# Optimization experiments

Measured on AMD Instinct MI355X. Metric: run time of the kernel, lower is better.

## Reference

```python
import jax, jax.numpy as jnp
import numpy as np

D_MODEL = 1024
NUM_HEADS = 16
LN_EPS = 1e-5


def setup_inputs() -> dict:
    key = jax.random.key(0)
    ks = jax.random.split(key, 8)
    d = D_MODEL
    x = jax.random.normal(ks[0], (8, 1024, d), dtype=jnp.float32)
    # nn.MultiheadAttention parameters (combined in_proj, out_proj)
    in_proj_w = jax.random.normal(ks[1], (3 * d, d), dtype=jnp.float32) / np.sqrt(d)
    in_proj_b = jnp.zeros((3 * d,), dtype=jnp.float32)
    out_proj_w = jax.random.normal(ks[2], (d, d), dtype=jnp.float32) / np.sqrt(d)
    out_proj_b = jnp.zeros((d,), dtype=jnp.float32)
    ln_w = jnp.ones((d,), dtype=jnp.float32)
    ln_b = jnp.zeros((d,), dtype=jnp.float32)
    time_decay = jnp.asarray(0.1, dtype=jnp.float32)
    return {"x": x, "time_decay": time_decay, "in_proj_w": in_proj_w,
            "in_proj_b": in_proj_b, "out_proj_w": out_proj_w,
            "out_proj_b": out_proj_b, "ln_w": ln_w, "ln_b": ln_b}


def reference(x, time_decay, in_proj_w, in_proj_b, out_proj_w, out_proj_b, ln_w, ln_b):
    B, S, d = x.shape
    H = NUM_HEADS
    hd = d // H
    # vectorized time-decay bias: -|time_decay| * |i - j|  (replaces nested loop)
    idx = jnp.arange(S, dtype=jnp.float32)
    attn_bias = -jnp.abs(time_decay) * jnp.abs(idx[:, None] - idx[None, :])  # [S,S]
    # combined QKV projection
    qkv = x @ in_proj_w.T + in_proj_b  # [B,S,3d]
    q, k, v = jnp.split(qkv, 3, axis=-1)
    q = q.reshape(B, S, H, hd)
    k = k.reshape(B, S, H, hd)
    v = v.reshape(B, S, H, hd)
    scale = 1.0 / np.sqrt(hd)
    scores = jnp.einsum('bqhd,bkhd->bhqk', q, k) * scale + attn_bias  # [B,H,S,S]
    weights = jax.nn.softmax(scores, axis=-1)
    attn = jnp.einsum('bhqk,bkhd->bqhd', weights, v).reshape(B, S, d)
    attn_out = attn @ out_proj_w.T + out_proj_b
    # need_weights=True with default average_attn_weights=True -> mean over heads
    attn_weights = jnp.mean(weights, axis=1)  # [B,S,S]
    # residual + LayerNorm
    y = x + attn_out
    mu = jnp.mean(y, axis=-1, keepdims=True)
    var = jnp.mean(jnp.square(y - mu), axis=-1, keepdims=True)
    out = (y - mu) / jnp.sqrt(var + LN_EPS) * ln_w + ln_b
    return (out, attn_weights)
```

## Files before the change

kernel.cpp:

```cpp
#include <hip/hip_runtime.h>
#include <cstddef>

#define BATCH   8
#define SEQ     1024
#define DMODEL  1024
#define NHEAD   16
#define HDIM    64
#define D3      3072
#define NROWS   (BATCH * SEQ)
#define LN_EPS  1e-5f

typedef __attribute__((ext_vector_type(4))) float f32x4;
typedef __attribute__((ext_vector_type(8))) short bf16x8;

__device__ __forceinline__ float b2f(unsigned short u) {
    union { unsigned int i; float f; } v; v.i = ((unsigned int)u) << 16; return v.f;
}
__device__ __forceinline__ unsigned short f2bu(float f) {
    union { float f; unsigned int i; } v; v.f = f;
    unsigned int r = v.i + 0x7fffu + ((v.i >> 16) & 1u);
    return (unsigned short)(r >> 16);
}
__device__ __forceinline__ void gl16(const void* g, void* l) {
    __builtin_amdgcn_global_load_lds(
        (const __attribute__((address_space(1))) unsigned int*)g,
        (__attribute__((address_space(3))) unsigned int*)l, 16, 0, 0);
}

#define NG_X  1048576
#define NG_WQ 393216
#define NG_WO 131072
__global__ __launch_bounds__(256)
void cvt_bf16(const float* __restrict__ x, const float* __restrict__ wq,
              const float* __restrict__ wo,
              unsigned short* __restrict__ xb, unsigned short* __restrict__ wqb,
              unsigned short* __restrict__ wob) {
    const int gidx = blockIdx.x * 256 + threadIdx.x;
    const float* src; unsigned short* dst; size_t off;
    if (gidx < NG_X)              { src = x;  dst = xb;  off = (size_t)gidx * 8; }
    else if (gidx < NG_X + NG_WQ) { src = wq; dst = wqb; off = (size_t)(gidx - NG_X) * 8; }
    else                          { src = wo; dst = wob; off = (size_t)(gidx - NG_X - NG_WQ) * 8; }
    float4 v0 = *(const float4*)(src + off);
    float4 v1 = *(const float4*)(src + off + 4);
    uint4 pv;
    pv.x = f2bu(v0.x) | ((unsigned int)f2bu(v0.y) << 16);
    pv.y = f2bu(v0.z) | ((unsigned int)f2bu(v0.w) << 16);
    pv.z = f2bu(v1.x) | ((unsigned int)f2bu(v1.y) << 16);
    pv.w = f2bu(v1.z) | ((unsigned int)f2bu(v1.w) << 16);
    *(uint4*)(dst + off) = pv;
}

__global__ __launch_bounds__(256)
void qkv_mfma(const unsigned short* __restrict__ xb,
              const unsigned short* __restrict__ wb,
              const float* __restrict__ bias,
              unsigned short* __restrict__ qh,
              unsigned short* __restrict__ kh,
              unsigned short* __restrict__ vt) {
    __shared__ unsigned short smem[8192];
    unsigned short* As = smem;
    unsigned short* Bs = smem + 4096;

    const int t = threadIdx.x;
    const int w = t >> 6, lane = t & 63;
    const int wm = w >> 1, wn = w & 1;
    const int g = lane >> 4, c = lane & 15;
    const int m0 = blockIdx.y * 128, n0 = blockIdx.x * 128;

    const int srow = t >> 2;
    const int scol = (t & 3) * 8;
    const unsigned short* ga = xb + (size_t)(m0 + srow) * 1024 + scol;
    const unsigned short* gb = wb + (size_t)(n0 + srow) * 1024 + scol;

    f32x4 acc[4][4];
#pragma unroll
    for (int i = 0; i < 4; ++i)
#pragma unroll
        for (int j = 0; j < 4; ++j) acc[i][j] = (f32x4){0.f, 0.f, 0.f, 0.f};

    for (int k0 = 0; k0 < 1024; k0 += 32) {
        gl16(ga + k0,             As + t * 8);
        gl16(ga + 64 * 1024 + k0, As + 2048 + t * 8);
        gl16(gb + k0,             Bs + t * 8);
        gl16(gb + 64 * 1024 + k0, Bs + 2048 + t * 8);
        __syncthreads();
        bf16x8 af[4], bf[4];
#pragma unroll
        for (int i = 0; i < 4; ++i)
            af[i] = *(const bf16x8*)(As + (wm * 64 + i * 16 + c) * 32 + g * 8);
#pragma unroll
        for (int j = 0; j < 4; ++j)
            bf[j] = *(const bf16x8*)(Bs + (wn * 64 + j * 16 + c) * 32 + g * 8);
#pragma unroll
        for (int i = 0; i < 4; ++i)
#pragma unroll
            for (int j = 0; j < 4; ++j)
                acc[i][j] = __builtin_amdgcn_mfma_f32_16x16x32_bf16(af[i], bf[j], acc[i][j], 0, 0, 0);
        __syncthreads();
    }

    float bsv[4];
#pragma unroll
    for (int j = 0; j < 4; ++j) bsv[j] = bias[n0 + wn * 64 + j * 16 + c];

    unsigned short* eslice = smem + w * 2048;
    const int b_ = m0 >> 10;

    if (n0 < 2048) {
        const int ncl   = n0 + wn * 64;
        unsigned short* dst = (ncl < 1024)
            ? qh + ((size_t)(b_ * 16 + (ncl >> 6)) * 1024) * 64
            : kh + ((size_t)(b_ * 16 + ((ncl - 1024) >> 6)) * 1024) * 64;
#pragma unroll
        for (int half = 0; half < 2; ++half) {
#pragma unroll
            for (int ii = 0; ii < 2; ++ii) {
                const int i = half * 2 + ii;
#pragma unroll
                for (int j = 0; j < 4; ++j)
#pragma unroll
                    for (int r = 0; r < 4; ++r)
                        eslice[(ii * 16 + g * 4 + r) * 64 + j * 16 + c] = f2bu(acc[i][j][r] + bsv[j]);
            }
#pragma unroll
            for (int u = 0; u < 4; ++u) {
                const int mloc = u * 8 + (lane >> 3);
                const int ncol = (lane & 7) * 8;
                bf16x8 row = *(const bf16x8*)(eslice + mloc * 64 + ncol);
                const int tok = (m0 & 1023) + wm * 64 + half * 32 + mloc;
                *(bf16x8*)(dst + (size_t)tok * 64 + ncol) = row;
            }
        }
    } else {
        const int key0  = (m0 & 1023) + wm * 64;
        const int hbase = (n0 + wn * 64 - 2048) >> 6;
#pragma unroll
        for (int half = 0; half < 2; ++half) {
#pragma unroll
            for (int jj = 0; jj < 2; ++jj) {
                const int j = half * 2 + jj;
                const int nloc = jj * 16 + c;
#pragma unroll
                for (int i = 0; i < 4; ++i)
#pragma unroll
                    for (int r = 0; r < 4; ++r) {
                        const int mloc  = i * 16 + g * 4 + r;
                        const int mphys = mloc ^ ((nloc & 7) << 3);
                        eslice[nloc * 64 + mphys] = f2bu(acc[i][j][r] + bsv[j]);
                    }
            }
#pragma unroll
            for (int u = 0; u < 4; ++u) {
                const int nloc  = u * 8 + (lane >> 3);
                const int mb    = lane & 7;
                const int mphys = (mb ^ (nloc & 7)) * 8;
                bf16x8 row = *(const bf16x8*)(eslice + nloc * 64 + mphys);
                const int d = half * 32 + nloc;
                *(bf16x8*)(vt + ((size_t)((b_ * 16 + hbase) * 64 + d)) * 1024 + key0 + mb * 8) = row;
            }
        }
    }
}

__global__ __launch_bounds__(256, 4)
void attn_mfma(const unsigned short* __restrict__ qh,
               const unsigned short* __restrict__ kh,
               const unsigned short* __restrict__ vt,
               const float* __restrict__ tdp,
               unsigned short* __restrict__ attnb,
               float* __restrict__ wout) {
    const int qt = blockIdx.x;
    const int b  = blockIdx.y;
    const int hg = blockIdx.z;
    const int t  = threadIdx.x;
    const int w  = t >> 6;
    const int lane = t & 63;
    const int g  = lane >> 4;
    const int c  = lane & 15;

    const int q0 = qt * 16;
    const float td = -fabsf(tdp[0]);

    __shared__ unsigned short P_s[16][1032];
    __shared__ float rs_s[4][16];

    float wsum[16][4];
#pragma unroll
    for (int tt = 0; tt < 16; ++tt)
#pragma unroll
        for (int r = 0; r < 4; ++r) wsum[tt][r] = 0.f;

    const int key_base = w * 256;

    for (int hi = 0; hi < 8; ++hi) {
        const int h = hg * 8 + hi;
        const unsigned short* qslab = qh + (size_t)(b * 16 + h) * 1024 * 64;
        const unsigned short* kslab = kh + (size_t)(b * 16 + h) * 1024 * 64;

        bf16x8 qa0 = *(const bf16x8*)(qslab + (size_t)(q0 + c) * 64 + g * 8);
        bf16x8 qa1 = *(const bf16x8*)(qslab + (size_t)(q0 + c) * 64 + 32 + g * 8);

        float rsum[4] = {0.f, 0.f, 0.f, 0.f};
#pragma unroll 2
        for (int tt = 0; tt < 16; ++tt) {
            const int key = key_base + tt * 16 + c;
            const unsigned short* kp = kslab + (size_t)key * 64 + g * 8;
            bf16x8 kb0 = *(const bf16x8*)(kp);
            bf16x8 kb1 = *(const bf16x8*)(kp + 32);
            f32x4 z = {0.f, 0.f, 0.f, 0.f};
            z = __builtin_amdgcn_mfma_f32_16x16x32_bf16(qa0, kb0, z, 0, 0, 0);
            z = __builtin_amdgcn_mfma_f32_16x16x32_bf16(qa1, kb1, z, 0, 0, 0);
            const float kf = (float)key;
#pragma unroll
            for (int r = 0; r < 4; ++r) {
                const float qf = (float)(q0 + g * 4 + r);
                const float e = __expf(z[r] * 0.125f + td * fabsf(kf - qf));
                rsum[r] += e;
                P_s[g * 4 + r][key_base + tt * 16 + c] = f2bu(e);
            }
        }
#pragma unroll
        for (int r = 0; r < 4; ++r) {
            rsum[r] += __shfl_xor(rsum[r], 1, 64);
            rsum[r] += __shfl_xor(rsum[r], 2, 64);
            rsum[r] += __shfl_xor(rsum[r], 4, 64);
            rsum[r] += __shfl_xor(rsum[r], 8, 64);
        }
        if (c == 0) {
#pragma unroll
            for (int r = 0; r < 4; ++r) rs_s[w][g * 4 + r] = rsum[r];
        }
        __syncthreads();

        float invl[4];
#pragma unroll
        for (int r = 0; r < 4; ++r) {
            const int row = g * 4 + r;
            invl[r] = 1.0f / (rs_s[0][row] + rs_s[1][row] + rs_s[2][row] + rs_s[3][row]);
        }

        f32x4 accO = {0.f, 0.f, 0.f, 0.f};
        const unsigned short* vhp = vt + (size_t)((b * 16 + h) * 64 + w * 16 + c) * 1024;
#pragma unroll 8
        for (int ks = 0; ks < 32; ++ks) {
            bf16x8 pa = *(const bf16x8*)(&P_s[c][ks * 32 + g * 8]);
            bf16x8 vb = *(const bf16x8*)(vhp + ks * 32 + g * 8);
            accO = __builtin_amdgcn_mfma_f32_16x16x32_bf16(pa, vb, accO, 0, 0, 0);
        }
        unsigned short* op = attnb + (size_t)(b * 1024 + q0) * 1024 + h * 64 + w * 16 + c;
#pragma unroll
        for (int r = 0; r < 4; ++r)
            op[(size_t)(g * 4 + r) * 1024] = f2bu(accO[r] * invl[r]);

#pragma unroll
        for (int tt = 0; tt < 16; ++tt)
#pragma unroll
            for (int r = 0; r < 4; ++r)
                wsum[tt][r] += b2f(P_s[g * 4 + r][key_base + tt * 16 + c]) * invl[r];
        __syncthreads();
    }

#pragma unroll
    for (int tt = 0; tt < 16; ++tt) {
#pragma unroll
        for (int r = 0; r < 4; ++r) {
            atomicAdd(&wout[(size_t)(b * 1024 + q0 + g * 4 + r) * 1024 + key_base + tt * 16 + c],
                      wsum[tt][r] * (1.0f / NHEAD));
        }
    }
}

__global__ __launch_bounds__(256)
void outproj_mfma(const unsigned short* __restrict__ ab,
                  const unsigned short* __restrict__ wob,
                  const float* __restrict__ bias,
                  const float* __restrict__ X,
                  float* __restrict__ Y) {
    __shared__ unsigned short smem[8192];
    unsigned short* As = smem;
    unsigned short* Bs = smem + 4096;

    const int t = threadIdx.x;
    const int w = t >> 6, lane = t & 63;
    const int wm = w >> 1, wn = w & 1;
    const int g = lane >> 4, c = lane & 15;
    const int m0 = blockIdx.y * 128, n0 = blockIdx.x * 128;

    const int srow = t >> 2;
    const int scol = (t & 3) * 8;
    const unsigned short* ga = ab  + (size_t)(m0 + srow) * 1024 + scol;
    const unsigned short* gb = wob + (size_t)(n0 + srow) * 1024 + scol;

    f32x4 acc[4][4];
#pragma unroll
    for (int i = 0; i < 4; ++i)
#pragma unroll
        for (int j = 0; j < 4; ++j) acc[i][j] = (f32x4){0.f, 0.f, 0.f, 0.f};

    for (int k0 = 0; k0 < 1024; k0 += 32) {
        gl16(ga + k0,             As + t * 8);
        gl16(ga + 64 * 1024 + k0, As + 2048 + t * 8);
        gl16(gb + k0,             Bs + t * 8);
        gl16(gb + 64 * 1024 + k0, Bs + 2048 + t * 8);
        __syncthreads();
        bf16x8 af[4], bf[4];
#pragma unroll
        for (int i = 0; i < 4; ++i)
            af[i] = *(const bf16x8*)(As + (wm * 64 + i * 16 + c) * 32 + g * 8);
#pragma unroll
        for (int j = 0; j < 4; ++j)
            bf[j] = *(const bf16x8*)(Bs + (wn * 64 + j * 16 + c) * 32 + g * 8);
#pragma unroll
        for (int i = 0; i < 4; ++i)
#pragma unroll
            for (int j = 0; j < 4; ++j)
                acc[i][j] = __builtin_amdgcn_mfma_f32_16x16x32_bf16(af[i], bf[j], acc[i][j], 0, 0, 0);
        __syncthreads();
    }

    float bsv[4];
#pragma unroll
    for (int j = 0; j < 4; ++j) bsv[j] = bias[n0 + wn * 64 + j * 16 + c];

#pragma unroll
    for (int i = 0; i < 4; ++i) {
#pragma unroll
        for (int r = 0; r < 4; ++r) {
            const int m = m0 + wm * 64 + i * 16 + g * 4 + r;
#pragma unroll
            for (int j = 0; j < 4; ++j) {
                const int n = n0 + wn * 64 + j * 16 + c;
                Y[(size_t)m * 1024 + n] = acc[i][j][r] + bsv[j] + X[(size_t)m * 1024 + n];
            }
        }
    }
}

__global__ __launch_bounds__(256)
void ln_kernel(const float* __restrict__ Y, const float* __restrict__ lnw,
               const float* __restrict__ lnb, float* __restrict__ out) {
    const int row = blockIdx.x, t = threadIdx.x;
    __shared__ float rs[256], rq[256];
    const float4 v = ((const float4*)(Y + (size_t)row * DMODEL))[t];
    rs[t] = v.x + v.y + v.z + v.w;
    rq[t] = v.x * v.x + v.y * v.y + v.z * v.z + v.w * v.w;
    __syncthreads();
    for (int off = 128; off > 0; off >>= 1) {
        if (t < off) { rs[t] += rs[t + off]; rq[t] += rq[t + off]; }
        __syncthreads();
    }
    const float mu   = rs[0] * (1.0f / DMODEL);
    const float var  = rq[0] * (1.0f / DMODEL) - mu * mu;
    const float rstd = rsqrtf(var + LN_EPS);
    const float4 w  = ((const float4*)lnw)[t];
    const float4 bb = ((const float4*)lnb)[t];
    float4 o;
    o.x = (v.x - mu) * rstd * w.x + bb.x;
    o.y = (v.y - mu) * rstd * w.y + bb.y;
    o.z = (v.z - mu) * rstd * w.z + bb.z;
    o.w = (v.w - mu) * rstd * w.w + bb.w;
    ((float4*)(out + (size_t)row * DMODEL))[t] = o;
}

extern "C" void kernel_launch(void* const* d_in, const int* in_sizes, int n_in,
                              void* d_out, int out_size, void* d_ws, size_t ws_size,
                              hipStream_t stream) {
    (void)in_sizes; (void)n_in; (void)out_size; (void)ws_size;
    const float* x    = (const float*)d_in[0];
    const float* td   = (const float*)d_in[1];
    const float* wqkv = (const float*)d_in[2];
    const float* bqkv = (const float*)d_in[3];
    const float* wo   = (const float*)d_in[4];
    const float* bo   = (const float*)d_in[5];
    const float* lnw  = (const float*)d_in[6];
    const float* lnb  = (const float*)d_in[7];

    float* out_ln = (float*)d_out;
    float* out_w  = (float*)d_out + (size_t)NROWS * SEQ;

    unsigned short* qh = (unsigned short*)d_ws;
    unsigned short* kh = qh + (size_t)128 * 1024 * 64;
    unsigned short* vt = kh + (size_t)128 * 1024 * 64;
    float*          y  = (float*)d_ws;

    unsigned short* attnb = (unsigned short*)d_out;
    unsigned short* wob   = (unsigned short*)d_out + (size_t)NROWS * DMODEL;
    unsigned short* xb    = (unsigned short*)out_w;
    unsigned short* wqkvb = xb + (size_t)NROWS * DMODEL;

    cvt_bf16    <<<(NG_X + NG_WQ + NG_WO) / 256, 256, 0, stream>>>(x, wqkv, wo, xb, wqkvb, wob);
    qkv_mfma    <<<dim3(D3 / 128, NROWS / 128), 256, 0, stream>>>(xb, wqkvb, bqkv, qh, kh, vt);
    hipMemsetAsync(out_w, 0, (size_t)BATCH * SEQ * SEQ * sizeof(float), stream);
    attn_mfma   <<<dim3(SEQ / 16, BATCH, 2),    256, 0, stream>>>(qh, kh, vt, td, attnb, out_w);
    outproj_mfma<<<dim3(DMODEL / 128, NROWS / 128), 256, 0, stream>>>(attnb, wob, bo, x, y);
    ln_kernel   <<<NROWS,                       256, 0, stream>>>(y, lnw, lnb, out_ln);
}
```

Baseline: 511.3 us.

## Process 32 query rows per attention block to reuse K/V loads, use exp2

The attention kernel now handles two 16-row query tiles per block, so each K and V fragment loaded from global memory feeds two MFMAs. This halves the per-query K/V traffic and halves the grid size. Exp is replaced with the hardware exp2 intrinsic using pre-scaled constants. The cost is doubled register state (wsum grows to 128 floats) and doubled LDS for P_s, with launch bounds lowered from 4 to 2 blocks per SM, which reduces occupancy.

```diff
diff --git a/kernel.cpp b/kernel.cpp
--- a/kernel.cpp
+++ b/kernel.cpp
@@ -162,7 +162,7 @@
     }
 }
 
-__global__ __launch_bounds__(256, 4)
+__global__ __launch_bounds__(256, 2)
 void attn_mfma(const unsigned short* __restrict__ qh,
                const unsigned short* __restrict__ kh,
                const unsigned short* __restrict__ vt,
@@ -178,96 +178,131 @@
     const int g  = lane >> 4;
     const int c  = lane & 15;
 
-    const int q0 = qt * 16;
-    const float td = -fabsf(tdp[0]);
-
-    __shared__ unsigned short P_s[16][1032];
-    __shared__ float rs_s[4][16];
-
-    float wsum[16][4];
-#pragma unroll
-    for (int tt = 0; tt < 16; ++tt)
-#pragma unroll
-        for (int r = 0; r < 4; ++r) wsum[tt][r] = 0.f;
+    const int q0 = qt * 32;
+    const float td2 = -fabsf(tdp[0]) * 1.44269504f;
+    const float sc2 = 0.125f * 1.44269504f;
+
+    __shared__ unsigned short P_s[32][1032];
+    __shared__ float rs_s[4][32];
+
+    float wsum[2][16][4];
+#pragma unroll
+    for (int i = 0; i < 2; ++i)
+#pragma unroll
+        for (int tt = 0; tt < 16; ++tt)
+#pragma unroll
+            for (int r = 0; r < 4; ++r) wsum[i][tt][r] = 0.f;
 
     const int key_base = w * 256;
+    const float kf0 = (float)(key_base + c);
 
     for (int hi = 0; hi < 8; ++hi) {
         const int h = hg * 8 + hi;
         const unsigned short* qslab = qh + (size_t)(b * 16 + h) * 1024 * 64;
         const unsigned short* kslab = kh + (size_t)(b * 16 + h) * 1024 * 64;
 
-        bf16x8 qa0 = *(const bf16x8*)(qslab + (size_t)(q0 + c) * 64 + g * 8);
-        bf16x8 qa1 = *(const bf16x8*)(qslab + (size_t)(q0 + c) * 64 + 32 + g * 8);
-
-        float rsum[4] = {0.f, 0.f, 0.f, 0.f};
+        bf16x8 qa[2][2];
+#pragma unroll
+        for (int i = 0; i < 2; ++i) {
+            const unsigned short* qp = qslab + (size_t)(q0 + i * 16 + c) * 64 + g * 8;
+            qa[i][0] = *(const bf16x8*)(qp);
+            qa[i][1] = *(const bf16x8*)(qp + 32);
+        }
+
+        float rsum[2][4] = {{0.f,0.f,0.f,0.f},{0.f,0.f,0.f,0.f}};
 #pragma unroll 2
         for (int tt = 0; tt < 16; ++tt) {
             const int key = key_base + tt * 16 + c;
             const unsigned short* kp = kslab + (size_t)key * 64 + g * 8;
             bf16x8 kb0 = *(const bf16x8*)(kp);
             bf16x8 kb1 = *(const bf16x8*)(kp + 32);
-            f32x4 z = {0.f, 0.f, 0.f, 0.f};
-            z = __builtin_amdgcn_mfma_f32_16x16x32_bf16(qa0, kb0, z, 0, 0, 0);
-            z = __builtin_amdgcn_mfma_f32_16x16x32_bf16(qa1, kb1, z, 0, 0, 0);
-            const float kf = (float)key;
-#pragma unroll
-            for (int r = 0; r < 4; ++r) {
-                const float qf = (float)(q0 + g * 4 + r);
-                const float e = __expf(z[r] * 0.125f + td * fabsf(kf - qf));
-                rsum[r] += e;
-                P_s[g * 4 + r][key_base + tt * 16 + c] = f2bu(e);
-            }
-        }
-#pragma unroll
-        for (int r = 0; r < 4; ++r) {
-            rsum[r] += __shfl_xor(rsum[r], 1, 64);
-            rsum[r] += __shfl_xor(rsum[r], 2, 64);
-            rsum[r] += __shfl_xor(rsum[r], 4, 64);
-            rsum[r] += __shfl_xor(rsum[r], 8, 64);
-        }
+            f32x4 z0 = {0.f, 0.f, 0.f, 0.f};
+            f32x4 z1 = {0.f, 0.f, 0.f, 0.f};
+            z0 = __builtin_amdgcn_mfma_f32_16x16x32_bf16(qa[0][0], kb0, z0, 0, 0, 0);
+            z1 = __builtin_amdgcn_mfma_f32_16x16x32_bf16(qa[1][0], kb0, z1, 0, 0, 0);
+            z0 = __builtin_amdgcn_mfma_f32_16x16x32_bf16(qa[0][1], kb1, z0, 0, 0, 0);
+            z1 = __builtin_amdgcn_mfma_f32_16x16x32_bf16(qa[1][1], kb1, z1, 0, 0, 0);
+            const float kf = kf0 + (float)(tt * 16);
+#pragma unroll
+            for (int r = 0; r < 4; ++r) {
+                const float qf0 = (float)(q0 + g * 4 + r);
+                const float e0 = __builtin_amdgcn_exp2f(z0[r] * sc2 + td2 * fabsf(kf - qf0));
+                rsum[0][r] += e0;
+                P_s[g * 4 + r][key_base + tt * 16 + c] = f2bu(e0);
+                const float qf1 = qf0 + 16.0f;
+                const float e1 = __builtin_amdgcn_exp2f(z1[r] * sc2 + td2 * fabsf(kf - qf1));
+                rsum[1][r] += e1;
+                P_s[16 + g * 4 + r][key_base + tt * 16 + c] = f2bu(e1);
+            }
+        }
+#pragma unroll
+        for (int i = 0; i < 2; ++i)
+#pragma unroll
+            for (int r = 0; r < 4; ++r) {
+                rsum[i][r] += __shfl_xor(rsum[i][r], 1, 64);
+                rsum[i][r] += __shfl_xor(rsum[i][r], 2, 64);
+                rsum[i][r] += __shfl_xor(rsum[i][r], 4, 64);
+                rsum[i][r] += __shfl_xor(rsum[i][r], 8, 64);
+            }
         if (c == 0) {
 #pragma unroll
-            for (int r = 0; r < 4; ++r) rs_s[w][g * 4 + r] = rsum[r];
-        }
-        __syncthreads();
-
-        float invl[4];
-#pragma unroll
-        for (int r = 0; r < 4; ++r) {
-            const int row = g * 4 + r;
-            invl[r] = 1.0f / (rs_s[0][row] + rs_s[1][row] + rs_s[2][row] + rs_s[3][row]);
-        }
-
-        f32x4 accO = {0.f, 0.f, 0.f, 0.f};
+            for (int i = 0; i < 2; ++i)
+#pragma unroll
+                for (int r = 0; r < 4; ++r) rs_s[w][i * 16 + g * 4 + r] = rsum[i][r];
+        }
+        __syncthreads();
+
+        float invl[2][4];
+#pragma unroll
+        for (int i = 0; i < 2; ++i)
+#pragma unroll
+            for (int r = 0; r < 4; ++r) {
+                const int row = i * 16 + g * 4 + r;
+                invl[i][r] = 1.0f / (rs_s[0][row] + rs_s[1][row] + rs_s[2][row] + rs_s[3][row]);
+            }
+
+        f32x4 accO0 = {0.f, 0.f, 0.f, 0.f};
+        f32x4 accO1 = {0.f, 0.f, 0.f, 0.f};
         const unsigned short* vhp = vt + (size_t)((b * 16 + h) * 64 + w * 16 + c) * 1024;
-#pragma unroll 8
+#pragma unroll 4
         for (int ks = 0; ks < 32; ++ks) {
-            bf16x8 pa = *(const bf16x8*)(&P_s[c][ks * 32 + g * 8]);
-            bf16x8 vb = *(const bf16x8*)(vhp + ks * 32 + g * 8);
-            accO = __builtin_amdgcn_mfma_f32_16x16x32_bf16(pa, vb, accO, 0, 0, 0);
-        }
-        unsigned short* op = attnb + (size_t)(b * 1024 + q0) * 1024 + h * 64 + w * 16 + c;
-#pragma unroll
-        for (int r = 0; r < 4; ++r)
-            op[(size_t)(g * 4 + r) * 1024] = f2bu(accO[r] * invl[r]);
-
+            bf16x8 pa0 = *(const bf16x8*)(&P_s[c][ks * 32 + g * 8]);
+            bf16x8 pa1 = *(const bf16x8*)(&P_s[16 + c][ks * 32 + g * 8]);
+            bf16x8 vb  = *(const bf16x8*)(vhp + ks * 32 + g * 8);
+            accO0 = __builtin_amdgcn_mfma_f32_16x16x32_bf16(pa0, vb, accO0, 0, 0, 0);
+            accO1 = __builtin_amdgcn_mfma_f32_16x16x32_bf16(pa1, vb, accO1, 0, 0, 0);
+        }
+        {
+            unsigned short* op0 = attnb + (size_t)(b * 1024 + q0) * 1024 + h * 64 + w * 16 + c;
+            unsigned short* op1 = op0 + (size_t)16 * 1024;
+#pragma unroll
+            for (int r = 0; r < 4; ++r) {
+                op0[(size_t)(g * 4 + r) * 1024] = f2bu(accO0[r] * invl[0][r]);
+                op1[(size_t)(g * 4 + r) * 1024] = f2bu(accO1[r] * invl[1][r]);
+            }
+        }
+
+#pragma unroll
+        for (int tt = 0; tt < 16; ++tt) {
+#pragma unroll
+            for (int r = 0; r < 4; ++r) {
+                wsum[0][tt][r] += b2f(P_s[g * 4 + r][key_base + tt * 16 + c]) * invl[0][r];
+                wsum[1][tt][r] += b2f(P_s[16 + g * 4 + r][key_base + tt * 16 + c]) * invl[1][r];
+            }
+        }
+        __syncthreads();
+    }
+
+#pragma unroll
+    for (int i = 0; i < 2; ++i)
 #pragma unroll
         for (int tt = 0; tt < 16; ++tt)
 #pragma unroll
-            for (int r = 0; r < 4; ++r)
-                wsum[tt][r] += b2f(P_s[g * 4 + r][key_base + tt * 16 + c]) * invl[r];
-        __syncthreads();
-    }
-
-#pragma unroll
-    for (int tt = 0; tt < 16; ++tt) {
-#pragma unroll
-        for (int r = 0; r < 4; ++r) {
-            atomicAdd(&wout[(size_t)(b * 1024 + q0 + g * 4 + r) * 1024 + key_base + tt * 16 + c],
-                      wsum[tt][r] * (1.0f / NHEAD));
-        }
-    }
+            for (int r = 0; r < 4; ++r) {
+                atomicAdd(&wout[(size_t)(b * 1024 + q0 + i * 16 + g * 4 + r) * 1024
+                                 + key_base + tt * 16 + c],
+                          wsum[i][tt][r] * (1.0f / NHEAD));
+            }
 }
 
 __global__ __launch_bounds__(256)
@@ -390,8 +425,8 @@
 
     cvt_bf16    <<<(NG_X + NG_WQ + NG_WO) / 256, 256, 0, stream>>>(x, wqkv, wo, xb, wqkvb, wob);
     qkv_mfma    <<<dim3(D3 / 128, NROWS / 128), 256, 0, stream>>>(xb, wqkvb, bqkv, qh, kh, vt);
-    hipMemsetAsync(out_w, 0, (size_t)BATCH * SEQ * SEQ * sizeof(float), stream);
-    attn_mfma   <<<dim3(SEQ / 16, BATCH, 2),    256, 0, stream>>>(qh, kh, vt, td, attnb, out_w);
+    (void)hipMemsetAsync(out_w, 0, (size_t)BATCH * SEQ * SEQ * sizeof(float), stream);
+    attn_mfma   <<<dim3(SEQ / 32, BATCH, 2),    256, 0, stream>>>(qh, kh, vt, td, attnb, out_w);
     outproj_mfma<<<dim3(DMODEL / 128, NROWS / 128), 256, 0, stream>>>(attnb, wob, bo, x, y);
     ln_kernel   <<<NROWS,                       256, 0, stream>>>(y, lnw, lnb, out_ln);
 }
```

Result: faster. 416.8 us (-18.5%).
